# Performance work log

Hardware: AMD Instinct MI355X
Metric: run time of the kernel (lower is better)

Reference implementation:

```python
import jax, jax.numpy as jnp
import numpy as np

GRID = 14
N_HEADS = 12
TOP_K = 32


def _valid_indices(grid):
    """Replicates create_locality_mask: cls row/col always valid; patch pairs
    valid iff Chebyshev distance on the grid <= 2 (includes diagonal)."""
    n = grid * grid + 1
    mask = np.zeros((n, n), dtype=bool)
    mask[0, :] = True
    mask[:, 0] = True
    idx = np.arange(grid * grid)
    r, c = idx // grid, idx % grid
    cheb = np.maximum(np.abs(r[:, None] - r[None, :]), np.abs(c[:, None] - c[None, :]))
    mask[1:, 1:] = cheb <= 2
    i_idx, j_idx = np.nonzero(mask)
    return jnp.asarray(i_idx, dtype=jnp.int32), jnp.asarray(j_idx, dtype=jnp.int32)

I_IDX, J_IDX = _valid_indices(GRID)  # nv = 4489 valid (query, key) pairs


def setup_inputs() -> dict:
    key = jax.random.key(0)
    ks = jax.random.split(key, 6)
    B, L, D = 32, GRID * GRID + 1, 768
    s = 0.02
    return {
        "x": jax.random.normal(ks[0], (B, L, D), jnp.float32),
        "W_q": jax.random.normal(ks[1], (D, D), jnp.float32) * s,
        "b_q": jnp.zeros((D,), jnp.float32),
        "W_k": jax.random.normal(ks[2], (D, D), jnp.float32) * s,
        "b_k": jnp.zeros((D,), jnp.float32),
        "W_v": jax.random.normal(ks[3], (D, D), jnp.float32) * s,
        "b_v": jnp.zeros((D,), jnp.float32),
        "W_o": jax.random.normal(ks[4], (D, D), jnp.float32) * s,
        "b_o": jnp.zeros((D,), jnp.float32),
        "log_sigma": jnp.zeros((), jnp.float32),  # sigma = 1.0
    }


def reference(x, W_q, b_q, W_k, b_k, W_v, b_v, W_o, b_o, log_sigma):
    B, L, D = x.shape
    H, dk = N_HEADS, D // N_HEADS

    def proj(W, b):
        y = jnp.einsum('bld,de->ble', x, W) + b
        return y.reshape(B, L, H, dk).transpose(0, 2, 1, 3)  # [B,H,L,dk]

    Q, K, V = proj(W_q, b_q), proj(W_k, b_k), proj(W_v, b_v)

    sigma_sq = jnp.exp(2.0 * log_sigma)
    # gather valid (i,j) pairs; nv pairs from the locality mask
    q_valid = Q[:, :, I_IDX, :]                       # [B,H,nv,dk]
    k_valid = K[:, :, J_IDX, :]                       # [B,H,nv,dk]
    dist_sq = jnp.sum((q_valid - k_valid) ** 2, axis=-1)  # [B,H,nv]
    scores_valid = (-0.5 / sigma_sq) * dist_sq

    neg_inf = jnp.array(-jnp.inf, x.dtype)
    scores = jnp.full((B, H, L, L), neg_inf, dtype=x.dtype)
    scores = scores.at[:, :, I_IDX, J_IDX].set(scores_valid)

    k_top = min(TOP_K, L)
    _, top_idx = jax.lax.top_k(scores, k_top)          # [B,H,L,k]
    bb = jnp.arange(B)[:, None, None, None]
    hh = jnp.arange(H)[None, :, None, None]
    nn = jnp.arange(L)[None, None, :, None]
    topk_mask = jnp.zeros((B, H, L, L), bool).at[bb, hh, nn, top_idx].set(True)

    final_mask = jnp.isfinite(scores) & topk_mask
    scores = jnp.where(final_mask, scores, neg_inf)
    weights = jax.nn.softmax(scores, axis=-1)          # [B,H,L,L]
    attention_mask = (weights > 1e-6).astype(x.dtype)

    consensus = jnp.einsum('bhij,bhjd->bhid', weights, V)
    consensus = consensus.transpose(0, 2, 1, 3).reshape(B, L, D)
    out = jnp.einsum('bld,de->ble', consensus, W_o) + b_o
    return out, weights, attention_mask
```

## Files before the change

kernel.cpp:

```cpp
#include <hip/hip_runtime.h>
#include <hip/hip_bf16.h>
#include <math.h>

#define GRIDN 14
#define L 197
#define H 12
#define DK 64
#define D 768
#define B 32
#define BL (B*L)
#define TOPK 32
#define NBH (B*H)
#define NROW (NBH*L)
#define QKV_ELEMS ((size_t)NROW*DK)
#define KSTR 68

typedef __attribute__((ext_vector_type(8))) short short8;
typedef __attribute__((ext_vector_type(4))) float floatx4;

__device__ __forceinline__ void load_lds16(void* lds, const void* g) {
    __builtin_amdgcn_global_load_lds(
        (const __attribute__((address_space(1))) unsigned int*)g,
        (__attribute__((address_space(3))) unsigned int*)lds, 16, 0, 0);
}

__global__ __launch_bounds__(256)
void prep(const float* __restrict__ x,
          const float* __restrict__ Wq, const float* __restrict__ Wk,
          const float* __restrict__ Wv, const float* __restrict__ Wo,
          __hip_bfloat16* __restrict__ xh, __hip_bfloat16* __restrict__ xl,
          __hip_bfloat16* __restrict__ WqTh, __hip_bfloat16* __restrict__ WqTl,
          __hip_bfloat16* __restrict__ WkTh, __hip_bfloat16* __restrict__ WkTl,
          __hip_bfloat16* __restrict__ WvT,  __hip_bfloat16* __restrict__ WoT)
{
    const int z = blockIdx.z;
    if (z == 4) {
        int lin = (blockIdx.y * 24 + blockIdx.x) * 256 + threadIdx.x;
        for (int i = lin; i < BL * D / 4; i += 24 * 24 * 256) {
            float4 v = ((const float4*)x)[i];
            union { __hip_bfloat16 b[4]; short4 s; } hh, ll;
            float f[4] = {v.x, v.y, v.z, v.w};
            #pragma unroll
            for (int j = 0; j < 4; ++j) {
                __hip_bfloat16 h = __float2bfloat16(f[j]);
                hh.b[j] = h;
                ll.b[j] = __float2bfloat16(f[j] - __bfloat162float(h));
            }
            ((short4*)xh)[i] = hh.s;
            ((short4*)xl)[i] = ll.s;
        }
        return;
    }
    __shared__ float tile[32][33];
    const float* src = (z == 0) ? Wq : (z == 1) ? Wk : (z == 2) ? Wv : Wo;
    __hip_bfloat16* dh = (z == 0) ? WqTh : (z == 1) ? WkTh : (z == 2) ? WvT : WoT;
    __hip_bfloat16* dl = (z == 0) ? WqTl : (z == 1) ? WkTl : nullptr;
    const int k0 = blockIdx.y * 32, n0 = blockIdx.x * 32;
    const int tx = threadIdx.x & 31, ty = threadIdx.x >> 5;

    for (int r = ty; r < 32; r += 8)
        tile[r][tx] = src[(size_t)(k0 + r) * D + n0 + tx];
    __syncthreads();
    for (int r = ty; r < 32; r += 8) {
        float v = tile[tx][r];
        __hip_bfloat16 h = __float2bfloat16(v);
        dh[(size_t)(n0 + r) * D + k0 + tx] = h;
        if (dl) dl[(size_t)(n0 + r) * D + k0 + tx] =
            __float2bfloat16(v - __bfloat162float(h));
    }
}

__global__ __launch_bounds__(256)
void gemm_qkv(const __hip_bfloat16* __restrict__ xh, const __hip_bfloat16* __restrict__ xl,
              const __hip_bfloat16* __restrict__ Wqh, const __hip_bfloat16* __restrict__ Wql,
              const __hip_bfloat16* __restrict__ Wkh, const __hip_bfloat16* __restrict__ Wkl,
              const __hip_bfloat16* __restrict__ Wvh,
              const float* __restrict__ bq, const float* __restrict__ bk,
              const float* __restrict__ bv,
              float* __restrict__ Qb, float* __restrict__ Kb, float* __restrict__ Vb)
{
    __shared__ __attribute__((aligned(16))) __hip_bfloat16 Ash[128 * 32];
    __shared__ __attribute__((aligned(16))) __hip_bfloat16 Bsh[128 * 32];
    __shared__ __attribute__((aligned(16))) __hip_bfloat16 Asl[128 * 32];
    __shared__ __attribute__((aligned(16))) __hip_bfloat16 Bsl[128 * 32];

    const int grp = blockIdx.y / 6, nt = blockIdx.y % 6;
    const __hip_bfloat16 *Bth, *Btl; const float* bias; float* C;
    if (grp == 0)      { Bth = Wqh; Btl = Wql; bias = bq; C = Qb; }
    else if (grp == 1) { Bth = Wkh; Btl = Wkl; bias = bk; C = Kb; }
    else               { Bth = Wvh; Btl = nullptr; bias = bv; C = Vb; }
    const bool split = (grp < 2);

    const int tid = threadIdx.x;
    const int wave = tid >> 6, lane = tid & 63;
    const int quad = lane >> 4, l16 = lane & 15;
    const int m0 = blockIdx.x * 128, n0 = nt * 128;
    const int wm = (wave & 1) * 64, wn = (wave >> 1) * 64;

    floatx4 acc[4][4] = {};

    int s_r[2], s_cs[2];
    #pragma unroll
    for (int u = 0; u < 2; ++u) {
        int idx = tid + u * 256;
        s_r[u] = idx >> 2; s_cs[u] = idx & 3;
    }

    for (int k0 = 0; k0 < D; k0 += 32) {
        #pragma unroll
        for (int u = 0; u < 2; ++u) {
            int r = s_r[u];
            int csrc = s_cs[u] ^ ((r >> 1) & 3);
            int gm = m0 + r; if (gm >= BL) gm = BL - 1;
            size_t aoff = (size_t)gm * D + k0 + csrc * 8;
            size_t boff = (size_t)(n0 + r) * D + k0 + csrc * 8;
            int lds_off = (wave * 64 + u * 256) * 16;
            load_lds16((char*)Ash + lds_off, xh + aoff);
            load_lds16((char*)Bsh + lds_off, Bth + boff);
            if (split) {
                load_lds16((char*)Asl + lds_off, xl + aoff);
                load_lds16((char*)Bsl + lds_off, Btl + boff);
            }
        }
        __syncthreads();

        short8 ah[4], bh[4];
        #pragma unroll
        for (int a = 0; a < 4; ++a) {
            int r = wm + a * 16 + l16;
            int slot = (r << 2) + (quad ^ ((r >> 1) & 3));
            ah[a] = *(const short8*)((const char*)Ash + (slot << 4));
        }
        #pragma unroll
        for (int b2 = 0; b2 < 4; ++b2) {
            int r = wn + b2 * 16 + l16;
            int slot = (r << 2) + (quad ^ ((r >> 1) & 3));
            bh[b2] = *(const short8*)((const char*)Bsh + (slot << 4));
        }
        if (split) {
            short8 al[4], bl[4];
            #pragma unroll
            for (int a = 0; a < 4; ++a) {
                int r = wm + a * 16 + l16;
                int slot = (r << 2) + (quad ^ ((r >> 1) & 3));
                al[a] = *(const short8*)((const char*)Asl + (slot << 4));
            }
            #pragma unroll
            for (int b2 = 0; b2 < 4; ++b2) {
                int r = wn + b2 * 16 + l16;
                int slot = (r << 2) + (quad ^ ((r >> 1) & 3));
                bl[b2] = *(const short8*)((const char*)Bsl + (slot << 4));
            }
            #pragma unroll
            for (int a = 0; a < 4; ++a)
                #pragma unroll
                for (int b2 = 0; b2 < 4; ++b2) {
                    acc[a][b2] = __builtin_amdgcn_mfma_f32_16x16x32_bf16(
                        al[a], bh[b2], acc[a][b2], 0, 0, 0);
                    acc[a][b2] = __builtin_amdgcn_mfma_f32_16x16x32_bf16(
                        ah[a], bl[b2], acc[a][b2], 0, 0, 0);
                }
        }
        #pragma unroll
        for (int a = 0; a < 4; ++a)
            #pragma unroll
            for (int b2 = 0; b2 < 4; ++b2)
                acc[a][b2] = __builtin_amdgcn_mfma_f32_16x16x32_bf16(
                    ah[a], bh[b2], acc[a][b2], 0, 0, 0);
        __syncthreads();
    }

    #pragma unroll
    for (int b2 = 0; b2 < 4; ++b2) {
        int n = n0 + wn + b2 * 16 + l16;
        float bvv = bias[n];
        int hh = n >> 6, dd = n & 63;
        #pragma unroll
        for (int a = 0; a < 4; ++a) {
            #pragma unroll
            for (int r = 0; r < 4; ++r) {
                int m = m0 + wm + a * 16 + quad * 4 + r;
                if (m < BL) {
                    int bb = m / L, ll = m % L;
                    C[((((size_t)bb * H + hh) * L + ll) << 6) + dd] =
                        acc[a][b2][r] + bvv;
                }
            }
        }
    }
}

__global__ __launch_bounds__(256)
void gemm_o(const __hip_bfloat16* __restrict__ A,
            const __hip_bfloat16* __restrict__ Bt,
            const float* __restrict__ bias, float* __restrict__ C)
{
    __shared__ __attribute__((aligned(16))) __hip_bfloat16 As[128 * 32];
    __shared__ __attribute__((aligned(16))) __hip_bfloat16 Bts[128 * 32];

    const int tid = threadIdx.x;
    const int wave = tid >> 6, lane = tid & 63;
    const int quad = lane >> 4, l16 = lane & 15;
    const int m0 = blockIdx.x * 128, n0 = blockIdx.y * 128;
    const int wm = (wave & 1) * 64, wn = (wave >> 1) * 64;

    floatx4 acc[4][4] = {};

    int s_r[2], s_cs[2];
    #pragma unroll
    for (int u = 0; u < 2; ++u) {
        int idx = tid + u * 256;
        s_r[u] = idx >> 2; s_cs[u] = idx & 3;
    }

    for (int k0 = 0; k0 < D; k0 += 32) {
        #pragma unroll
        for (int u = 0; u < 2; ++u) {
            int r = s_r[u];
            int csrc = s_cs[u] ^ ((r >> 1) & 3);
            int gm = m0 + r; if (gm >= BL) gm = BL - 1;
            int lds_off = (wave * 64 + u * 256) * 16;
            load_lds16((char*)As + lds_off, A + (size_t)gm * D + k0 + csrc * 8);
            load_lds16((char*)Bts + lds_off, Bt + (size_t)(n0 + r) * D + k0 + csrc * 8);
        }
        __syncthreads();

        short8 af[4], bf[4];
        #pragma unroll
        for (int a = 0; a < 4; ++a) {
            int r = wm + a * 16 + l16;
            int slot = (r << 2) + (quad ^ ((r >> 1) & 3));
            af[a] = *(const short8*)((const char*)As + (slot << 4));
        }
        #pragma unroll
        for (int b2 = 0; b2 < 4; ++b2) {
            int r = wn + b2 * 16 + l16;
            int slot = (r << 2) + (quad ^ ((r >> 1) & 3));
            bf[b2] = *(const short8*)((const char*)Bts + (slot << 4));
        }
        #pragma unroll
        for (int a = 0; a < 4; ++a)
            #pragma unroll
            for (int b2 = 0; b2 < 4; ++b2)
                acc[a][b2] = __builtin_amdgcn_mfma_f32_16x16x32_bf16(
                    af[a], bf[b2], acc[a][b2], 0, 0, 0);
        __syncthreads();
    }

    #pragma unroll
    for (int b2 = 0; b2 < 4; ++b2) {
        int n = n0 + wn + b2 * 16 + l16;
        float bvv = bias[n];
        #pragma unroll
        for (int a = 0; a < 4; ++a) {
            #pragma unroll
            for (int r = 0; r < 4; ++r) {
                int m = m0 + wm + a * 16 + quad * 4 + r;
                if (m < BL) C[(size_t)m * D + n] = acc[a][b2][r] + bvv;
            }
        }
    }
}

__global__ __launch_bounds__(512)
void attn_fused(const float* __restrict__ Q, const float* __restrict__ Kg,
                const float* __restrict__ Vg, const float* __restrict__ logsig,
                float* __restrict__ wout, float* __restrict__ mout,
                __hip_bfloat16* __restrict__ cons)
{
    __shared__ __attribute__((aligned(16))) float KV[L * KSTR];
    __shared__ float qbuf[8][64];
    __shared__ float clsbuf[L];
    __shared__ float wjW[99][32];
    __shared__ unsigned char wjJ[99][32];
    __shared__ unsigned int winA[L];
    __shared__ unsigned int winB[L];
    __shared__ unsigned char joff[76];

    const int bh = blockIdx.x;
    const int yb = blockIdx.y;
    const int b = bh / H, h = bh % H;
    const int tid = threadIdx.x, wave = tid >> 6, lane = tid & 63;
    const int base_i = yb * 99;
    const int half = lane & 1;

    if (tid >= 1 && tid < L) {
        int r = (tid - 1) / GRIDN, c = (tid - 1) % GRIDN;
        int r0 = r - 2 < 0 ? 0 : r - 2, r1 = r + 2 > 13 ? 13 : r + 2;
        int c0 = c - 2 < 0 ? 0 : c - 2, c1 = c + 2 > 13 ? 13 : c + 2;
        int Wd = c1 - c0 + 1, Hh = r1 - r0 + 1;
        winA[tid] = (unsigned)r0 | ((unsigned)c0 << 8) |
                    ((unsigned)Wd << 16) | ((unsigned)Hh << 24);
        winB[tid] = (unsigned)(Hh * Wd + 1) |
                    ((unsigned)(1 + r0 * GRIDN + c0) << 8);
    }
    if (tid == 0) { winA[0] = 0; winB[0] = 0; }
    if (tid < 75) {
        int w = tid / 25 + 3, tm = tid % 25;
        joff[tid] = (unsigned char)((tm / w) * GRIDN + tm % w);
    }

    int pr4[4], pc4[4];
    #pragma unroll
    for (int k = 0; k < 4; ++k) {
        int p = lane + (k << 6);
        if (p >= 1 && p < L) { pr4[k] = (p - 1) / GRIDN; pc4[k] = (p - 1) % GRIDN; }
        else                 { pr4[k] = 255; pc4[k] = 255; }
    }

    const float* Kp = Kg + (size_t)bh * L * DK;
    for (int idx = tid; idx < L * 16; idx += 512) {
        int r = idx >> 4, c4 = idx & 15;
        *(float4*)&KV[r * KSTR + c4 * 4] = *(const float4*)&Kp[r * 64 + c4 * 4];
    }
    __syncthreads();

    const float coef = -0.5f * expf(-2.0f * logsig[0]);
    const int starts0[9] = {0, 9, 22, 35, 48, 61, 74, 87, 99};
    const int starts1[9] = {99, 112, 124, 136, 148, 161, 173, 185, 197};
    const int i_begin = yb ? starts1[wave] : starts0[wave];
    const int i_end   = yb ? starts1[wave + 1] : starts0[wave + 1];

    float qreg = (i_begin < i_end)
               ? Q[((size_t)bh * L + i_begin) * 64 + lane] : 0.f;

    for (int i = i_begin; i < i_end; ++i) {
        const int rowid = bh * L + i;
        const size_t wb = (size_t)rowid * L;
        const int local = i - base_i;

        qbuf[wave][lane] = qreg;
        if (i + 1 < i_end)
            qreg = Q[((size_t)rowid + 1) * 64 + lane];

        if (i == 0) {
            const float4* qp = (const float4*)&qbuf[wave][half << 5];
            for (int p = 0; p < 7; ++p) {
                int t = (p << 5) + (lane >> 1);
                bool valid = t < L;
                float s = 0.f;
                if (valid) {
                    const float4* kp = (const float4*)&KV[t * KSTR + (half << 5)];
                    #pragma unroll
                    for (int d4 = 0; d4 < 8; ++d4) {
                        float4 qv = qp[d4], kv = kp[d4];
                        float dx = qv.x - kv.x, dy = qv.y - kv.y;
                        float dz = qv.z - kv.z, dw = qv.w - kv.w;
                        s += dx * dx + dy * dy + dz * dz + dw * dw;
                    }
                }
                s += __shfl_xor(s, 1);
                if (valid && !half) clsbuf[t] = coef * s;
            }
            float orig[4], cur[4]; int selb = 0;
            #pragma unroll
            for (int k = 0; k < 4; ++k) {
                int t = lane + (k << 6);
                float v = (t < L) ? clsbuf[t] : -INFINITY;
                orig[k] = v; cur[k] = v;
            }
            float gmax = -INFINITY;
            for (int it = 0; it < TOPK; ++it) {
                float bv = cur[0]; int bt = lane;
                #pragma unroll
                for (int k = 1; k < 4; ++k)
                    if (cur[k] > bv) { bv = cur[k]; bt = lane + (k << 6); }
                #pragma unroll
                for (int off = 32; off; off >>= 1) {
                    float ov = __shfl_xor(bv, off);
                    int   ot = __shfl_xor(bt, off);
                    if (ov > bv || (ov == bv && ot < bt)) { bv = ov; bt = ot; }
                }
                if (it == 0) gmax = bv;
                if ((bt & 63) == lane) { cur[bt >> 6] = -INFINITY; selb |= 1 << (bt >> 6); }
            }
            float zl = 0.f; float wk[4];
            #pragma unroll
            for (int k = 0; k < 4; ++k) {
                wk[k] = ((selb >> k) & 1) ? expf(orig[k] - gmax) : 0.f;
                zl += wk[k];
            }
            #pragma unroll
            for (int off = 32; off; off >>= 1) zl += __shfl_xor(zl, off);

            #pragma unroll
            for (int k = 0; k < 4; ++k) {
                int p = lane + (k << 6);
                if (p < L) {
                    float wv = wk[k] / zl;
                    wout[wb + p] = wv;
                    mout[wb + p] = (wv > 1e-6f) ? 1.f : 0.f;
                }
            }
            int slot = 0;
            #pragma unroll
            for (int k = 0; k < 4; ++k) {
                bool sel = (selb >> k) & 1;
                unsigned long long mk = __ballot(sel);
                if (sel) {
                    int tt = slot + (int)__popcll(mk & ((1ull << lane) - 1ull));
                    wjW[0][tt] = wk[k] / zl;
                    wjJ[0][tt] = (unsigned char)(lane + (k << 6));
                }
                slot += (int)__popcll(mk);
            }
        } else {
            const unsigned wa = winA[i], wbp = winB[i];
            const int r0 = wa & 255, c0 = (wa >> 8) & 255;
            const int Wd2 = (wa >> 16) & 255, Hh = wa >> 24;
            const int n = wbp & 255, jbase = wbp >> 8;

            int t = lane >> 1;
            bool valid = t < n;
            float s = 0.f; int j = 0;
            if (valid) {
                if (t > 0) j = jbase + joff[(Wd2 - 3) * 25 + (t - 1)];
                const float4* kp = (const float4*)&KV[j * KSTR + (half << 5)];
                const float4* qp = (const float4*)&qbuf[wave][half << 5];
                #pragma unroll
                for (int d4 = 0; d4 < 8; ++d4) {
                    float4 qv = qp[d4], kv = kp[d4];
                    float dx = qv.x - kv.x, dy = qv.y - kv.y;
                    float dz = qv.z - kv.z, dw = qv.w - kv.w;
                    s += dx * dx + dy * dy + dz * dz + dw * dw;
                }
            }
            s += __shfl_xor(s, 1);
            float sc = valid ? coef * s : -INFINITY;

            float mx = sc;
            #pragma unroll
            for (int off = 32; off; off >>= 1) mx = fmaxf(mx, __shfl_xor(mx, off));
            float e = valid ? expf(sc - mx) : 0.f;
            float es = half ? 0.f : e;
            #pragma unroll
            for (int off = 32; off; off >>= 1) es += __shfl_xor(es, off);
            float wv = e / es;

            if (!half) {
                float wcv = valid ? wv : 0.f;
                wjW[local][t] = wcv;
                wjJ[local][t] = (unsigned char)(valid ? j : 0);
            }
            #pragma unroll
            for (int k = 0; k < 4; ++k) {
                int p = lane + (k << 6);
                if (p < L) {
                    float wd = 0.f;
                    if (p == 0) wd = wjW[local][0];
                    else {
                        unsigned du = (unsigned)(pr4[k] - r0);
                        unsigned dv = (unsigned)(pc4[k] - c0);
                        if (du < (unsigned)Hh && dv < (unsigned)Wd2)
                            wd = wjW[local][1 + du * Wd2 + dv];
                    }
                    wout[wb + p] = wd;
                    mout[wb + p] = (wd > 1e-6f) ? 1.f : 0.f;
                }
            }
        }
    }
    __syncthreads();

    const float* Vp = Vg + (size_t)bh * L * DK;
    for (int idx = tid; idx < L * 16; idx += 512) {
        int r = idx >> 4, c4 = idx & 15;
        *(float4*)&KV[r * KSTR + c4 * 4] = *(const float4*)&Vp[r * 64 + c4 * 4];
    }
    __syncthreads();

    const int cstarts0[9] = {0, 13, 26, 38, 50, 62, 74, 87, 99};
    const int c_begin = yb ? starts1[wave] : cstarts0[wave];
    const int c_end   = yb ? starts1[wave + 1] : cstarts0[wave + 1];

    for (int i = c_begin; i < c_end; ++i) {
        const int local = i - base_i;
        float acc = 0.f;
        #pragma unroll
        for (int t = 0; t < 32; ++t) {
            float w = wjW[local][t];
            int j = wjJ[local][t];
            acc += w * KV[j * KSTR + lane];
        }
        cons[((size_t)b * L + i) * D + h * 64 + lane] = __float2bfloat16(acc);
    }
}

extern "C" void kernel_launch(void* const* d_in, const int* in_sizes, int n_in,
                              void* d_out, int out_size, void* d_ws, size_t ws_size,
                              hipStream_t stream)
{
    const float* x   = (const float*)d_in[0];
    const float* Wq  = (const float*)d_in[1];
    const float* bq  = (const float*)d_in[2];
    const float* Wk  = (const float*)d_in[3];
    const float* bk  = (const float*)d_in[4];
    const float* Wv  = (const float*)d_in[5];
    const float* bv  = (const float*)d_in[6];
    const float* Wo  = (const float*)d_in[7];
    const float* bo  = (const float*)d_in[8];
    const float* lsg = (const float*)d_in[9];

    float* out  = (float*)d_out;
    float* wout = out + QKV_ELEMS;
    float* mout = wout + (size_t)B * H * L * L;

    float* Qb  = (float*)d_ws;
    float* Kb  = Qb + QKV_ELEMS;
    float* Vb  = Kb + QKV_ELEMS;
    __hip_bfloat16* xh = (__hip_bfloat16*)(Vb + QKV_ELEMS);
    __hip_bfloat16* xl = xh + (size_t)BL * D;
    __hip_bfloat16* WqTh = xl + (size_t)BL * D;
    __hip_bfloat16* WqTl = WqTh + (size_t)D * D;
    __hip_bfloat16* WkTh = WqTl + (size_t)D * D;
    __hip_bfloat16* WkTl = WkTh + (size_t)D * D;
    __hip_bfloat16* WvT  = WkTl + (size_t)D * D;
    __hip_bfloat16* WoT  = WvT  + (size_t)D * D;
    __hip_bfloat16* consb = xh;

    prep<<<dim3(24, 24, 5), 256, 0, stream>>>(
        x, Wq, Wk, Wv, Wo, xh, xl, WqTh, WqTl, WkTh, WkTl, WvT, WoT);

    gemm_qkv<<<dim3(50, 18), 256, 0, stream>>>(
        xh, xl, WqTh, WqTl, WkTh, WkTl, WvT, bq, bk, bv, Qb, Kb, Vb);

    attn_fused<<<dim3(NBH, 2), 512, 0, stream>>>(
        Qb, Kb, Vb, lsg, wout, mout, consb);

    gemm_o<<<dim3(50, 6), 256, 0, stream>>>(consb, WoT, bo, out);
}
```

Before: 333.6 us.

## Move weights-times-V into separate dense MFMA kernel reading dense weight output

```diff
diff --git a/kernel.cpp b/kernel.cpp
--- a/kernel.cpp
+++ b/kernel.cpp
@@ -262,26 +262,93 @@
     }
 }
 
+__global__ __launch_bounds__(256)
+void gemm_cons(const float* __restrict__ Vg, const float* __restrict__ Wd,
+               __hip_bfloat16* __restrict__ cons)
+{
+    __shared__ __attribute__((aligned(16))) __hip_bfloat16 Vt[64 * 224];
+    __shared__ __attribute__((aligned(16))) __hip_bfloat16 Aw[208 * 32];
+
+    const int bh = blockIdx.x;
+    const int b = bh / H, h = bh % H;
+    const int tid = threadIdx.x, wave = tid >> 6, lane = tid & 63;
+    const int quad = lane >> 4, l16 = lane & 15;
+
+    for (int e = tid; e < 64 * 224 / 8; e += 256)
+        *(short8*)&Vt[e * 8] = short8{0,0,0,0,0,0,0,0};
+    __syncthreads();
+    const float* Vp = Vg + (size_t)bh * L * DK;
+    for (int idx = tid; idx < L * 16; idx += 256) {
+        int j = idx >> 4, d4 = (idx & 15) * 4;
+        float4 v = *(const float4*)&Vp[j * 64 + d4];
+        Vt[(d4 + 0) * 224 + j] = __float2bfloat16(v.x);
+        Vt[(d4 + 1) * 224 + j] = __float2bfloat16(v.y);
+        Vt[(d4 + 2) * 224 + j] = __float2bfloat16(v.z);
+        Vt[(d4 + 3) * 224 + j] = __float2bfloat16(v.w);
+    }
+
+    floatx4 acc[4][4] = {};
+    const size_t wbase = (size_t)bh * L * L;
+
+    for (int kc = 0; kc < 7; ++kc) {
+        __syncthreads();
+        for (int e = tid; e < 208 * 32; e += 256) {
+            int r = e >> 5, k = e & 31;
+            float w = Wd[wbase + (size_t)r * L + kc * 32 + k];
+            Aw[e] = __float2bfloat16(w);
+        }
+        __syncthreads();
+
+        short8 bf4[4];
+        #pragma unroll
+        for (int nt = 0; nt < 4; ++nt)
+            bf4[nt] = *(const short8*)&Vt[(nt * 16 + l16) * 224 + kc * 32 + quad * 8];
+        #pragma unroll
+        for (int sl = 0; sl < 4; ++sl) {
+            int mt = wave + sl * 4;
+            if (mt < 13) {
+                short8 af = *(const short8*)&Aw[(mt * 16 + l16) * 32 + quad * 8];
+                #pragma unroll
+                for (int nt = 0; nt < 4; ++nt)
+                    acc[sl][nt] = __builtin_amdgcn_mfma_f32_16x16x32_bf16(
+                        af, bf4[nt], acc[sl][nt], 0, 0, 0);
+            }
+        }
+    }
+
+    #pragma unroll
+    for (int sl = 0; sl < 4; ++sl) {
+        int mt = wave + sl * 4;
+        if (mt >= 13) continue;
+        #pragma unroll
+        for (int nt = 0; nt < 4; ++nt) {
+            #pragma unroll
+            for (int r = 0; r < 4; ++r) {
+                int i = mt * 16 + quad * 4 + r;
+                if (i < L)
+                    cons[((size_t)b * L + i) * D + h * 64 + nt * 16 + l16] =
+                        __float2bfloat16(acc[sl][nt][r]);
+            }
+        }
+    }
+}
+
 __global__ __launch_bounds__(512)
 void attn_fused(const float* __restrict__ Q, const float* __restrict__ Kg,
-                const float* __restrict__ Vg, const float* __restrict__ logsig,
-                float* __restrict__ wout, float* __restrict__ mout,
-                __hip_bfloat16* __restrict__ cons)
+                const float* __restrict__ logsig,
+                float* __restrict__ wout, float* __restrict__ mout)
 {
     __shared__ __attribute__((aligned(16))) float KV[L * KSTR];
     __shared__ float qbuf[8][64];
+    __shared__ float ws[8][32];
     __shared__ float clsbuf[L];
-    __shared__ float wjW[99][32];
-    __shared__ unsigned char wjJ[99][32];
     __shared__ unsigned int winA[L];
     __shared__ unsigned int winB[L];
     __shared__ unsigned char joff[76];
 
     const int bh = blockIdx.x;
     const int yb = blockIdx.y;
-    const int b = bh / H, h = bh % H;
     const int tid = threadIdx.x, wave = tid >> 6, lane = tid & 63;
-    const int base_i = yb * 99;
     const int half = lane & 1;
 
     if (tid >= 1 && tid < L) {
@@ -327,7 +394,6 @@
     for (int i = i_begin; i < i_end; ++i) {
         const int rowid = bh * L + i;
         const size_t wb = (size_t)rowid * L;
-        const int local = i - base_i;
 
         qbuf[wave][lane] = qreg;
         if (i + 1 < i_end)
@@ -392,18 +458,6 @@
                     mout[wb + p] = (wv > 1e-6f) ? 1.f : 0.f;
                 }
             }
-            int slot = 0;
-            #pragma unroll
-            for (int k = 0; k < 4; ++k) {
-                bool sel = (selb >> k) & 1;
-                unsigned long long mk = __ballot(sel);
-                if (sel) {
-                    int tt = slot + (int)__popcll(mk & ((1ull << lane) - 1ull));
-                    wjW[0][tt] = wk[k] / zl;
-                    wjJ[0][tt] = (unsigned char)(lane + (k << 6));
-                }
-                slot += (int)__popcll(mk);
-            }
         } else {
             const unsigned wa = winA[i], wbp = winB[i];
             const int r0 = wa & 255, c0 = (wa >> 8) & 255;
@@ -437,52 +491,25 @@
             for (int off = 32; off; off >>= 1) es += __shfl_xor(es, off);
             float wv = e / es;
 
-            if (!half) {
-                float wcv = valid ? wv : 0.f;
-                wjW[local][t] = wcv;
-                wjJ[local][t] = (unsigned char)(valid ? j : 0);
-            }
+            if (!half) ws[wave][t] = valid ? wv : 0.f;
+
             #pragma unroll
             for (int k = 0; k < 4; ++k) {
                 int p = lane + (k << 6);
                 if (p < L) {
                     float wd = 0.f;
-                    if (p == 0) wd = wjW[local][0];
+                    if (p == 0) wd = ws[wave][0];
                     else {
                         unsigned du = (unsigned)(pr4[k] - r0);
                         unsigned dv = (unsigned)(pc4[k] - c0);
                         if (du < (unsigned)Hh && dv < (unsigned)Wd2)
-                            wd = wjW[local][1 + du * Wd2 + dv];
+                            wd = ws[wave][1 + du * Wd2 + dv];
                     }
                     wout[wb + p] = wd;
                     mout[wb + p] = (wd > 1e-6f) ? 1.f : 0.f;
                 }
             }
         }
-    }
-    __syncthreads();
-
-    const float* Vp = Vg + (size_t)bh * L * DK;
-    for (int idx = tid; idx < L * 16; idx += 512) {
-        int r = idx >> 4, c4 = idx & 15;
-        *(float4*)&KV[r * KSTR + c4 * 4] = *(const float4*)&Vp[r * 64 + c4 * 4];
-    }
-    __syncthreads();
-
-    const int cstarts0[9] = {0, 13, 26, 38, 50, 62, 74, 87, 99};
-    const int c_begin = yb ? starts1[wave] : cstarts0[wave];
-    const int c_end   = yb ? starts1[wave + 1] : cstarts0[wave + 1];
-
-    for (int i = c_begin; i < c_end; ++i) {
-        const int local = i - base_i;
-        float acc = 0.f;
-        #pragma unroll
-        for (int t = 0; t < 32; ++t) {
-            float w = wjW[local][t];
-            int j = wjJ[local][t];
-            acc += w * KV[j * KSTR + lane];
-        }
-        cons[((size_t)b * L + i) * D + h * 64 + lane] = __float2bfloat16(acc);
     }
 }
 
@@ -525,7 +552,9 @@
         xh, xl, WqTh, WqTl, WkTh, WkTl, WvT, bq, bk, bv, Qb, Kb, Vb);
 
     attn_fused<<<dim3(NBH, 2), 512, 0, stream>>>(
-        Qb, Kb, Vb, lsg, wout, mout, consb);
+        Qb, Kb, lsg, wout, mout);
+
+    gemm_cons<<<NBH, 256, 0, stream>>>(Vb, wout, consb);
 
     gemm_o<<<dim3(50, 6), 256, 0, stream>>>(consb, WoT, bo, out);
 }
```

New measurement: 348.4 us. +4.4%, slower.
